# Performance work log

Hardware: AMD Instinct MI355X
Metric: run time of the kernel (lower is better)

## Reference

```python
import jax, jax.numpy as jnp
import numpy as np

B, T, D, HD = 256, 256, 384, 64  # batch, seq_len, embedding_dim, head_dim


def setup_inputs() -> dict:
    key = jax.random.key(0)
    k1, k2, k3, k4 = jax.random.split(key, 4)
    x = jax.random.normal(k1, (B, T, D), dtype=jnp.float32)
    # nn.Linear(D, HD, bias=False) weight shape is [HD, D]; init scaled like kaiming-uniform magnitude
    Wq = jax.random.normal(k2, (HD, D), dtype=jnp.float32) * (1.0 / np.sqrt(D))
    Wk = jax.random.normal(k3, (HD, D), dtype=jnp.float32) * (1.0 / np.sqrt(D))
    Wv = jax.random.normal(k4, (HD, D), dtype=jnp.float32) * (1.0 / np.sqrt(D))
    return {"x": x, "Wq": Wq, "Wk": Wk, "Wv": Wv}


def reference(x, Wq, Wk, Wv):
    # Projections: x @ W^T  (Linear with bias=False)
    q = jnp.einsum('btd,hd->bth', x, Wq)  # [B,T,HD]
    k = jnp.einsum('btd,hd->bth', x, Wk)
    v = jnp.einsum('btd,hd->bth', x, Wv)
    scale = 1.0 / np.sqrt(HD).astype(np.float32)
    scores = jnp.einsum('bqh,bkh->bqk', q, k) * scale  # [B,T,T]
    T_ = x.shape[1]
    causal = jnp.tril(jnp.ones((T_, T_), dtype=bool))
    scores = jnp.where(causal, scores, jnp.float32(-jnp.inf))
    attn = jax.nn.softmax(scores, axis=-1)
    # dropout disabled (eval mode) for deterministic reference
    return jnp.einsum('bqk,bkh->bqh', attn, v)
```

## Files before the change

kernel.cpp:

```cpp
#include <hip/hip_runtime.h>

typedef __attribute__((ext_vector_type(8))) short bf16x8;
typedef __attribute__((ext_vector_type(4))) float f32x4;

__device__ inline unsigned short f2bf(float f) {
    unsigned u = __float_as_uint(f);
    return (unsigned short)((u + 0x7fffu + ((u >> 16) & 1u)) >> 16);
}

__device__ inline void gload16(const void* g, void* l) {
    __builtin_amdgcn_global_load_lds(
        (const __attribute__((address_space(1))) unsigned*)g,
        (__attribute__((address_space(3))) unsigned*)l, 16, 0, 0);
}

__global__ void wconv(const float* __restrict__ Wq, const float* __restrict__ Wk,
                      const float* __restrict__ Wv, short* __restrict__ Wp) {
    int i = blockIdx.x * 256 + threadIdx.x;
    if (i >= 192 * 384) return;
    int col = i / 384;
    int k   = i - col * 384;
    const float* src = col < 64 ? (Wq + col * 384)
                     : col < 128 ? (Wk + (col - 64) * 384)
                                 : (Wv + (col - 128) * 384);
    int kc = k >> 5, g = (k >> 3) & 3, kl = k & 7;
    Wp[kc * 6144 + (((g * 192 + col) ^ g) << 3) + kl] = (short)f2bf(src[k]);
}

__global__ __launch_bounds__(256, 2) void qkv_proj(
    const float* __restrict__ x, const short* __restrict__ Wp,
    short* __restrict__ Qw, short* __restrict__ Kw, short* __restrict__ Vw) {
    __shared__ unsigned char LDSRAW[57344];
    float* const xb0 = (float*)LDSRAW;
    float* const xb1 = xb0 + 4096;
    short* const wb0 = (short*)(LDSRAW + 32768);
    short* const wb1 = wb0 + 6144;

    const int tid = threadIdx.x;
    const int wv = tid >> 6, lane = tid & 63;
    const int g = lane >> 4, c = lane & 15;
    const int wm = (wv >> 1) * 64, wn = (wv & 1) * 96;
    const size_t m0 = (size_t)blockIdx.x * 128;

    f32x4 acc[4][6];
#pragma unroll
    for (int i = 0; i < 4; ++i)
#pragma unroll
        for (int j = 0; j < 6; ++j) acc[i][j] = (f32x4){0.f, 0.f, 0.f, 0.f};

    const int xrow8 = lane >> 3;
    const int xgcol = ((lane & 7) ^ xrow8) << 2;

#define STAGE_X(KC, XB)                                                       \
    {                                                                         \
        _Pragma("unroll")                                                     \
        for (int i_ = 0; i_ < 4; ++i_) {                                      \
            int seg = wv * 4 + i_;                                            \
            const float* gp = x + (m0 + seg * 8 + xrow8) * 384 + (KC) * 32 + xgcol; \
            gload16(gp, (XB) + seg * 256);                                    \
        }                                                                     \
    }
#define STAGE_W(KC, WB)                                                       \
    {                                                                         \
        _Pragma("unroll")                                                     \
        for (int i_ = 0; i_ < 3; ++i_) {                                      \
            int seg = wv * 3 + i_;                                            \
            const short* gp = Wp + (KC) * 6144 + seg * 512 + lane * 8;        \
            gload16(gp, (WB) + seg * 512);                                    \
        }                                                                     \
    }

    STAGE_X(0, xb0)
    STAGE_W(0, wb0)
    asm volatile("s_waitcnt vmcnt(0)" ::: "memory");
    __syncthreads();

    for (int s = 0; s < 12; ++s) {
        if (s < 11) {
            if (s & 1) { STAGE_X(s + 1, xb0) STAGE_W(s + 1, wb0) }
            else       { STAGE_X(s + 1, xb1) STAGE_W(s + 1, wb1) }
        }
        const float* xb = (s & 1) ? xb1 : xb0;
        const short* wb = (s & 1) ? wb1 : wb0;
        bf16x8 af[4], bfr[6];
#pragma unroll
        for (int mi = 0; mi < 4; ++mi) {
            const int row = wm + 16 * mi + c;
            const int rx = row & 7;
            f32x4 lo = *(const f32x4*)&xb[row * 32 + (((2 * g) ^ rx) << 2)];
            f32x4 hi = *(const f32x4*)&xb[row * 32 + (((2 * g + 1) ^ rx) << 2)];
            bf16x8 t;
            t[0] = (short)f2bf(lo[0]); t[1] = (short)f2bf(lo[1]);
            t[2] = (short)f2bf(lo[2]); t[3] = (short)f2bf(lo[3]);
            t[4] = (short)f2bf(hi[0]); t[5] = (short)f2bf(hi[1]);
            t[6] = (short)f2bf(hi[2]); t[7] = (short)f2bf(hi[3]);
            af[mi] = t;
        }
#pragma unroll
        for (int nj = 0; nj < 6; ++nj)
            bfr[nj] = *(const bf16x8*)&wb[((g * 192 + wn + 16 * nj + c) ^ g) << 3];
#pragma unroll
        for (int mi = 0; mi < 4; ++mi)
#pragma unroll
            for (int nj = 0; nj < 6; ++nj)
                acc[mi][nj] = __builtin_amdgcn_mfma_f32_16x16x32_bf16(
                    af[mi], bfr[nj], acc[mi][nj], 0, 0, 0);
        asm volatile("s_waitcnt vmcnt(0)" ::: "memory");
        __syncthreads();
    }

    short* ep = (short*)LDSRAW;
#pragma unroll
    for (int mi = 0; mi < 4; ++mi)
#pragma unroll
        for (int nj = 0; nj < 6; ++nj) {
            const int row = wm + 16 * mi + 4 * g;
#pragma unroll
            for (int r = 0; r < 4; ++r)
                ep[(row + r) * 192 + wn + 16 * nj + c] = (short)f2bf(acc[mi][nj][r]);
        }
    __syncthreads();
#pragma unroll
    for (int p = 0; p < 4; ++p) {
        int u = tid + 256 * p;
        int row = u >> 3, c8 = u & 7;
        *(uint4*)(Qw + (m0 + row) * 64 + c8 * 8) = *(const uint4*)&ep[row * 192 + c8 * 8];
        *(uint4*)(Kw + (m0 + row) * 64 + c8 * 8) = *(const uint4*)&ep[row * 192 + 64 + c8 * 8];
        *(uint4*)(Vw + (m0 + row) * 64 + c8 * 8) = *(const uint4*)&ep[row * 192 + 128 + c8 * 8];
    }
#undef STAGE_X
#undef STAGE_W
}

__global__ __launch_bounds__(512, 2) void attn_mfma(
    const short* __restrict__ Qw, const short* __restrict__ Kw,
    const short* __restrict__ Vw, float* __restrict__ out) {
    __shared__ short Ksh[256 * 72];
    __shared__ short Vt[64 * 264];
    __shared__ short Pb[8][640];
    const int tid = threadIdx.x;
    const int wv = tid >> 6, lane = tid & 63;
    const int g = lane >> 4, c = lane & 15;
    const int b = blockIdx.x;
    const short* Qg = Qw + b * 16384;
    const short* Kg = Kw + b * 16384;
    const short* Vg = Vw + b * 16384;

#pragma unroll
    for (int p = 0; p < 4; ++p) {
        int idx = tid + 512 * p;
        int r = idx >> 3, q8 = idx & 7;
        *(uint4*)&Ksh[r * 72 + q8 * 8] = *(const uint4*)(Kg + r * 64 + q8 * 8);
    }
#pragma unroll
    for (int p = 0; p < 4; ++p) {
        int idx = tid + 512 * p;
        int r = idx >> 3, q8 = idx & 7;
        uint4 v = *(const uint4*)(Vg + r * 64 + q8 * 8);
        unsigned vw[4] = {v.x, v.y, v.z, v.w};
        int swz = (q8 & 7) << 3;
#pragma unroll
        for (int w2 = 0; w2 < 4; ++w2) {
            int h0 = q8 * 8 + w2 * 2;
            Vt[((h0 + 0) * 264 + r) ^ swz] = (short)(vw[w2] & 0xffff);
            Vt[((h0 + 1) * 264 + r) ^ swz] = (short)(vw[w2] >> 16);
        }
    }
    __syncthreads();

    for (int half = 0; half < 2; ++half) {
        const int q0 = (half == 0) ? 16 * wv : 240 - 16 * wv;
        bf16x8 qf0 = *(const bf16x8*)(Qg + (q0 + c) * 64 + g * 8);
        bf16x8 qf1 = *(const bf16x8*)(Qg + (q0 + c) * 64 + 32 + g * 8);
        f32x4 o[4];
#pragma unroll
        for (int nj = 0; nj < 4; ++nj) o[nj] = (f32x4){0.f, 0.f, 0.f, 0.f};
        float m[4] = {-INFINITY, -INFINITY, -INFINITY, -INFINITY};
        float ls[4] = {0.f, 0.f, 0.f, 0.f};
        const int jmax = (q0 + 15) >> 5;

        for (int j = 0; j <= jmax; ++j) {
            f32x4 s0 = {0.f, 0.f, 0.f, 0.f}, s1 = {0.f, 0.f, 0.f, 0.f};
            {
                bf16x8 kf;
                kf = *(const bf16x8*)&Ksh[(32 * j + c) * 72 + g * 8];
                s0 = __builtin_amdgcn_mfma_f32_16x16x32_bf16(qf0, kf, s0, 0, 0, 0);
                kf = *(const bf16x8*)&Ksh[(32 * j + c) * 72 + 32 + g * 8];
                s0 = __builtin_amdgcn_mfma_f32_16x16x32_bf16(qf1, kf, s0, 0, 0, 0);
                kf = *(const bf16x8*)&Ksh[(32 * j + 16 + c) * 72 + g * 8];
                s1 = __builtin_amdgcn_mfma_f32_16x16x32_bf16(qf0, kf, s1, 0, 0, 0);
                kf = *(const bf16x8*)&Ksh[(32 * j + 16 + c) * 72 + 32 + g * 8];
                s1 = __builtin_amdgcn_mfma_f32_16x16x32_bf16(qf1, kf, s1, 0, 0, 0);
            }
            float t0[4], t1[4];
#pragma unroll
            for (int r = 0; r < 4; ++r) {
                t0[r] = s0[r] * 0.125f;
                t1[r] = s1[r] * 0.125f;
            }
            if (j == jmax) {
                int q = q0 + 4 * g;
#pragma unroll
                for (int r = 0; r < 4; ++r) {
                    if (32 * j + c > q + r) t0[r] = -INFINITY;
                    if (32 * j + 16 + c > q + r) t1[r] = -INFINITY;
                }
            }
            float corr[4], p0[4], p1[4];
#pragma unroll
            for (int r = 0; r < 4; ++r) {
                float v = fmaxf(t0[r], t1[r]);
#pragma unroll
                for (int off = 1; off < 16; off <<= 1) v = fmaxf(v, __shfl_xor(v, off, 16));
                float mn = fmaxf(m[r], v);
                corr[r] = __expf(m[r] - mn);
                m[r] = mn;
                p0[r] = __expf(t0[r] - mn);
                p1[r] = __expf(t1[r] - mn);
                float rs = p0[r] + p1[r];
#pragma unroll
                for (int off = 1; off < 16; off <<= 1) rs += __shfl_xor(rs, off, 16);
                ls[r] = ls[r] * corr[r] + rs;
            }
#pragma unroll
            for (int nj = 0; nj < 4; ++nj) {
                f32x4 t = o[nj];
                t[0] *= corr[0]; t[1] *= corr[1]; t[2] *= corr[2]; t[3] *= corr[3];
                o[nj] = t;
            }
            short* pb = Pb[wv];
#pragma unroll
            for (int r = 0; r < 4; ++r) {
                pb[(4 * g + r) * 40 + c]      = (short)f2bf(p0[r]);
                pb[(4 * g + r) * 40 + 16 + c] = (short)f2bf(p1[r]);
            }
            bf16x8 pfa = *(const bf16x8*)&pb[c * 40 + g * 8];
#pragma unroll
            for (int nj = 0; nj < 4; ++nj) {
                int h = 16 * nj + c;
                int swz = ((2 * nj + (c >> 3)) & 7) << 3;
                bf16x8 vf = *(const bf16x8*)&Vt[(h * 264 + 32 * j + g * 8) ^ swz];
                o[nj] = __builtin_amdgcn_mfma_f32_16x16x32_bf16(pfa, vf, o[nj], 0, 0, 0);
            }
        }
        float inv[4];
#pragma unroll
        for (int r = 0; r < 4; ++r) inv[r] = 1.f / ls[r];
        float* ob = out + ((size_t)b * 256 + q0) * 64;
#pragma unroll
        for (int nj = 0; nj < 4; ++nj)
#pragma unroll
            for (int r = 0; r < 4; ++r)
                ob[(4 * g + r) * 64 + 16 * nj + c] = o[nj][r] * inv[r];
    }
}

extern "C" void kernel_launch(void* const* d_in, const int* in_sizes, int n_in,
                              void* d_out, int out_size, void* d_ws, size_t ws_size,
                              hipStream_t stream) {
    const float* x  = (const float*)d_in[0];
    const float* Wq = (const float*)d_in[1];
    const float* Wk = (const float*)d_in[2];
    const float* Wv = (const float*)d_in[3];
    float* out = (float*)d_out;

    short* Qws = (short*)d_ws;
    short* Kws = Qws + (size_t)65536 * 64;
    short* Vws = Kws + (size_t)65536 * 64;
    short* Wp  = Vws + (size_t)65536 * 64;

    wconv<<<dim3(288), dim3(256), 0, stream>>>(Wq, Wk, Wv, Wp);
    qkv_proj<<<dim3(512), dim3(256), 0, stream>>>(x, Wp, Qws, Kws, Vws);
    attn_mfma<<<dim3(256), dim3(512), 0, stream>>>(Qws, Kws, Vws, out);
}
```

Before: 47.03 us.

## Preload whole bf16 x tile into LDS and halve projection row tile

```diff
diff --git a/kernel.cpp b/kernel.cpp
--- a/kernel.cpp
+++ b/kernel.cpp
@@ -30,77 +30,65 @@
 __global__ __launch_bounds__(256, 2) void qkv_proj(
     const float* __restrict__ x, const short* __restrict__ Wp,
     short* __restrict__ Qw, short* __restrict__ Kw, short* __restrict__ Vw) {
-    __shared__ unsigned char LDSRAW[57344];
-    float* const xb0 = (float*)LDSRAW;
-    float* const xb1 = xb0 + 4096;
-    short* const wb0 = (short*)(LDSRAW + 32768);
-    short* const wb1 = wb0 + 6144;
+    __shared__ short xs[64 * 392];
+    __shared__ short wst[2 * 6144];
 
     const int tid = threadIdx.x;
     const int wv = tid >> 6, lane = tid & 63;
     const int g = lane >> 4, c = lane & 15;
-    const int wm = (wv >> 1) * 64, wn = (wv & 1) * 96;
-    const size_t m0 = (size_t)blockIdx.x * 128;
-
-    f32x4 acc[4][6];
-#pragma unroll
-    for (int i = 0; i < 4; ++i)
-#pragma unroll
-        for (int j = 0; j < 6; ++j) acc[i][j] = (f32x4){0.f, 0.f, 0.f, 0.f};
-
-    const int xrow8 = lane >> 3;
-    const int xgcol = ((lane & 7) ^ xrow8) << 2;
-
-#define STAGE_X(KC, XB)                                                       \
-    {                                                                         \
-        _Pragma("unroll")                                                     \
-        for (int i_ = 0; i_ < 4; ++i_) {                                      \
-            int seg = wv * 4 + i_;                                            \
-            const float* gp = x + (m0 + seg * 8 + xrow8) * 384 + (KC) * 32 + xgcol; \
-            gload16(gp, (XB) + seg * 256);                                    \
-        }                                                                     \
-    }
-#define STAGE_W(KC, WB)                                                       \
+    const int wm = (wv >> 1) * 32, wn = (wv & 1) * 96;
+    const size_t m0 = (size_t)blockIdx.x * 64;
+
+#define STAGE_W(KC, BUF)                                                      \
     {                                                                         \
         _Pragma("unroll")                                                     \
         for (int i_ = 0; i_ < 3; ++i_) {                                      \
             int seg = wv * 3 + i_;                                            \
-            const short* gp = Wp + (KC) * 6144 + seg * 512 + lane * 8;        \
-            gload16(gp, (WB) + seg * 512);                                    \
+            gload16(Wp + (KC) * 6144 + seg * 512 + lane * 8,                  \
+                    wst + (BUF) * 6144 + seg * 512);                          \
         }                                                                     \
     }
 
-    STAGE_X(0, xb0)
-    STAGE_W(0, wb0)
+    f32x4 acc[2][6];
+#pragma unroll
+    for (int i = 0; i < 2; ++i)
+#pragma unroll
+        for (int j = 0; j < 6; ++j) acc[i][j] = (f32x4){0.f, 0.f, 0.f, 0.f};
+
+    STAGE_W(0, 0)
+    for (int batch = 0; batch < 3; ++batch) {
+        float4 t[8];
+#pragma unroll
+        for (int i = 0; i < 8; ++i) {
+            int u = tid + 256 * (batch * 8 + i);
+            int row = u / 96, c4 = u - row * 96;
+            t[i] = *(const float4*)(x + (m0 + row) * 384 + c4 * 4);
+        }
+#pragma unroll
+        for (int i = 0; i < 8; ++i) {
+            int u = tid + 256 * (batch * 8 + i);
+            int row = u / 96, c4 = u - row * 96;
+            uint2 p;
+            p.x = (unsigned)f2bf(t[i].x) | ((unsigned)f2bf(t[i].y) << 16);
+            p.y = (unsigned)f2bf(t[i].z) | ((unsigned)f2bf(t[i].w) << 16);
+            *(uint2*)&xs[row * 392 + c4 * 4] = p;
+        }
+    }
     asm volatile("s_waitcnt vmcnt(0)" ::: "memory");
     __syncthreads();
 
     for (int s = 0; s < 12; ++s) {
-        if (s < 11) {
-            if (s & 1) { STAGE_X(s + 1, xb0) STAGE_W(s + 1, wb0) }
-            else       { STAGE_X(s + 1, xb1) STAGE_W(s + 1, wb1) }
-        }
-        const float* xb = (s & 1) ? xb1 : xb0;
-        const short* wb = (s & 1) ? wb1 : wb0;
-        bf16x8 af[4], bfr[6];
-#pragma unroll
-        for (int mi = 0; mi < 4; ++mi) {
-            const int row = wm + 16 * mi + c;
-            const int rx = row & 7;
-            f32x4 lo = *(const f32x4*)&xb[row * 32 + (((2 * g) ^ rx) << 2)];
-            f32x4 hi = *(const f32x4*)&xb[row * 32 + (((2 * g + 1) ^ rx) << 2)];
-            bf16x8 t;
-            t[0] = (short)f2bf(lo[0]); t[1] = (short)f2bf(lo[1]);
-            t[2] = (short)f2bf(lo[2]); t[3] = (short)f2bf(lo[3]);
-            t[4] = (short)f2bf(hi[0]); t[5] = (short)f2bf(hi[1]);
-            t[6] = (short)f2bf(hi[2]); t[7] = (short)f2bf(hi[3]);
-            af[mi] = t;
-        }
+        if (s < 11) STAGE_W(s + 1, (s + 1) & 1)
+        const short* wb = wst + (s & 1) * 6144;
+        bf16x8 af[2], bfr[6];
+#pragma unroll
+        for (int mi = 0; mi < 2; ++mi)
+            af[mi] = *(const bf16x8*)&xs[(wm + 16 * mi + c) * 392 + s * 32 + g * 8];
 #pragma unroll
         for (int nj = 0; nj < 6; ++nj)
             bfr[nj] = *(const bf16x8*)&wb[((g * 192 + wn + 16 * nj + c) ^ g) << 3];
 #pragma unroll
-        for (int mi = 0; mi < 4; ++mi)
+        for (int mi = 0; mi < 2; ++mi)
 #pragma unroll
             for (int nj = 0; nj < 6; ++nj)
                 acc[mi][nj] = __builtin_amdgcn_mfma_f32_16x16x32_bf16(
@@ -109,9 +97,9 @@
         __syncthreads();
     }
 
-    short* ep = (short*)LDSRAW;
-#pragma unroll
-    for (int mi = 0; mi < 4; ++mi)
+    short* ep = wst;
+#pragma unroll
+    for (int mi = 0; mi < 2; ++mi)
 #pragma unroll
         for (int nj = 0; nj < 6; ++nj) {
             const int row = wm + 16 * mi + 4 * g;
@@ -121,14 +109,13 @@
         }
     __syncthreads();
 #pragma unroll
-    for (int p = 0; p < 4; ++p) {
+    for (int p = 0; p < 2; ++p) {
         int u = tid + 256 * p;
         int row = u >> 3, c8 = u & 7;
         *(uint4*)(Qw + (m0 + row) * 64 + c8 * 8) = *(const uint4*)&ep[row * 192 + c8 * 8];
         *(uint4*)(Kw + (m0 + row) * 64 + c8 * 8) = *(const uint4*)&ep[row * 192 + 64 + c8 * 8];
         *(uint4*)(Vw + (m0 + row) * 64 + c8 * 8) = *(const uint4*)&ep[row * 192 + 128 + c8 * 8];
     }
-#undef STAGE_X
 #undef STAGE_W
 }
 
@@ -270,6 +257,6 @@
     short* Wp  = Vws + (size_t)65536 * 64;
 
     wconv<<<dim3(288), dim3(256), 0, stream>>>(Wq, Wk, Wv, Wp);
-    qkv_proj<<<dim3(512), dim3(256), 0, stream>>>(x, Wp, Qws, Kws, Vws);
+    qkv_proj<<<dim3(1024), dim3(256), 0, stream>>>(x, Wp, Qws, Kws, Vws);
     attn_mfma<<<dim3(256), dim3(512), 0, stream>>>(Qws, Kws, Vws, out);
 }
```

After: 57.57 us. 1.22x slower.

## Triple-buffer x tiles and use partial vmcnt waits in QKV projection

Applied to the files above, without the earlier changes.

```diff
diff --git a/kernel.cpp b/kernel.cpp
--- a/kernel.cpp
+++ b/kernel.cpp
@@ -7,7 +7,6 @@
     unsigned u = __float_as_uint(f);
     return (unsigned short)((u + 0x7fffu + ((u >> 16) & 1u)) >> 16);
 }
-
 __device__ inline void gload16(const void* g, void* l) {
     __builtin_amdgcn_global_load_lds(
         (const __attribute__((address_space(1))) unsigned*)g,
@@ -30,11 +29,7 @@
 __global__ __launch_bounds__(256, 2) void qkv_proj(
     const float* __restrict__ x, const short* __restrict__ Wp,
     short* __restrict__ Qw, short* __restrict__ Kw, short* __restrict__ Vw) {
-    __shared__ unsigned char LDSRAW[57344];
-    float* const xb0 = (float*)LDSRAW;
-    float* const xb1 = xb0 + 4096;
-    short* const wb0 = (short*)(LDSRAW + 32768);
-    short* const wb1 = wb0 + 6144;
+    __shared__ unsigned char LDSRAW[73728];
 
     const int tid = threadIdx.x;
     const int wv = tid >> 6, lane = tid & 63;
@@ -42,46 +37,50 @@
     const int wm = (wv >> 1) * 64, wn = (wv & 1) * 96;
     const size_t m0 = (size_t)blockIdx.x * 128;
 
-    f32x4 acc[4][6];
-#pragma unroll
-    for (int i = 0; i < 4; ++i)
-#pragma unroll
-        for (int j = 0; j < 6; ++j) acc[i][j] = (f32x4){0.f, 0.f, 0.f, 0.f};
-
     const int xrow8 = lane >> 3;
     const int xgcol = ((lane & 7) ^ xrow8) << 2;
 
-#define STAGE_X(KC, XB)                                                       \
-    {                                                                         \
-        _Pragma("unroll")                                                     \
-        for (int i_ = 0; i_ < 4; ++i_) {                                      \
-            int seg = wv * 4 + i_;                                            \
+#define XBUF(I) ((float*)(LDSRAW + ((I) % 3) * 16384))
+#define WBUF(I) ((short*)(LDSRAW + 49152 + ((I) % 2) * 12288))
+#define STAGE_X(KC)                                                          \
+    {                                                                        \
+        float* xb_ = XBUF(KC);                                               \
+        _Pragma("unroll")                                                    \
+        for (int i_ = 0; i_ < 4; ++i_) {                                     \
+            int seg = wv * 4 + i_;                                           \
             const float* gp = x + (m0 + seg * 8 + xrow8) * 384 + (KC) * 32 + xgcol; \
-            gload16(gp, (XB) + seg * 256);                                    \
-        }                                                                     \
-    }
-#define STAGE_W(KC, WB)                                                       \
-    {                                                                         \
-        _Pragma("unroll")                                                     \
-        for (int i_ = 0; i_ < 3; ++i_) {                                      \
-            int seg = wv * 3 + i_;                                            \
-            const short* gp = Wp + (KC) * 6144 + seg * 512 + lane * 8;        \
-            gload16(gp, (WB) + seg * 512);                                    \
-        }                                                                     \
-    }
-
-    STAGE_X(0, xb0)
-    STAGE_W(0, wb0)
-    asm volatile("s_waitcnt vmcnt(0)" ::: "memory");
-    __syncthreads();
-
+            gload16(gp, xb_ + seg * 256);                                    \
+        }                                                                    \
+    }
+#define STAGE_W(KC)                                                          \
+    {                                                                        \
+        short* wb_ = WBUF(KC);                                               \
+        _Pragma("unroll")                                                    \
+        for (int i_ = 0; i_ < 3; ++i_) {                                     \
+            int seg = wv * 3 + i_;                                           \
+            gload16(Wp + (KC) * 6144 + seg * 512 + lane * 8, wb_ + seg * 512); \
+        }                                                                    \
+    }
+
+    f32x4 acc[4][6];
+#pragma unroll
+    for (int i = 0; i < 4; ++i)
+#pragma unroll
+        for (int j = 0; j < 6; ++j) acc[i][j] = (f32x4){0.f, 0.f, 0.f, 0.f};
+
+    STAGE_X(0)
+    STAGE_W(0)
+    STAGE_X(1)
+    asm volatile("s_waitcnt vmcnt(4)" ::: "memory");
+    __builtin_amdgcn_s_barrier();
+    __builtin_amdgcn_sched_barrier(0);
+
+#pragma unroll
     for (int s = 0; s < 12; ++s) {
-        if (s < 11) {
-            if (s & 1) { STAGE_X(s + 1, xb0) STAGE_W(s + 1, wb0) }
-            else       { STAGE_X(s + 1, xb1) STAGE_W(s + 1, wb1) }
-        }
-        const float* xb = (s & 1) ? xb1 : xb0;
-        const short* wb = (s & 1) ? wb1 : wb0;
+        if (s <= 10) STAGE_W(s + 1)
+        if (s <= 9)  STAGE_X(s + 2)
+        const float* xb = XBUF(s);
+        const short* wb = WBUF(s);
         bf16x8 af[4], bfr[6];
 #pragma unroll
         for (int mi = 0; mi < 4; ++mi) {
@@ -105,10 +104,13 @@
             for (int nj = 0; nj < 6; ++nj)
                 acc[mi][nj] = __builtin_amdgcn_mfma_f32_16x16x32_bf16(
                     af[mi], bfr[nj], acc[mi][nj], 0, 0, 0);
-        asm volatile("s_waitcnt vmcnt(0)" ::: "memory");
-        __syncthreads();
-    }
-
+        if (s <= 9)       asm volatile("s_waitcnt vmcnt(4)" ::: "memory");
+        else if (s == 10) asm volatile("s_waitcnt vmcnt(0)" ::: "memory");
+        __builtin_amdgcn_s_barrier();
+        __builtin_amdgcn_sched_barrier(0);
+    }
+
+    __syncthreads();
     short* ep = (short*)LDSRAW;
 #pragma unroll
     for (int mi = 0; mi < 4; ++mi)
@@ -130,6 +132,8 @@
     }
 #undef STAGE_X
 #undef STAGE_W
+#undef XBUF
+#undef WBUF
 }
 
 __global__ __launch_bounds__(512, 2) void attn_mfma(
```

Measured after the change: 47.07 us. About the same (+0.1%).
